# Optimization experiments

Hardware: AMD Instinct MI355X
Metric: run time of the kernel (lower is better)

The kernel has to match this reference:

```python
import jax, jax.numpy as jnp
import numpy as np


def _prelu(x, alpha):
    # PReLU with alpha shared over H,W (per-channel alpha, shape (C,))
    return jnp.where(x >= 0, x, alpha * x)


def _maxpool_2x2_s1_same(x):
    # TF MaxPooling2D(pool_size=2, strides=1, padding='same'): pad bottom/right
    return jax.lax.reduce_window(
        x, -jnp.inf, jax.lax.max,
        window_dimensions=(1, 2, 2, 1), window_strides=(1, 1, 1, 1),
        padding=[(0, 0), (0, 1), (0, 1), (0, 0)])


def _down_sample(x, W, b, alpha):
    # 1x1 Conv2D stride 2 'same' == subsample then channel matmul
    y = jnp.einsum('bhwc,cd->bhwd', x[:, ::2, ::2, :], W) + b
    y = _prelu(y, alpha)
    return _maxpool_2x2_s1_same(y)


def _up_sample(x, W, b, alpha):
    # 1x1 Conv2DTranspose stride 2 'same': even positions get conv output, rest only bias
    B, H, Wd, C = x.shape
    y = jnp.einsum('bhwc,cd->bhwd', x, W)
    z = jnp.zeros((B, 2 * H, 2 * Wd, C), dtype=x.dtype).at[:, ::2, ::2, :].set(y) + b
    z = _prelu(z, alpha)
    return _maxpool_2x2_s1_same(z)


def setup_inputs() -> dict:
    key = jax.random.key(0)
    ks = jax.random.split(key, 12)
    B, H, C = 8, 512, 3
    return {
        'input1': jax.random.normal(ks[0], (B, 2 * H, 2 * H, C), jnp.float32),
        'input2': jax.random.normal(ks[1], (B, H, H, C), jnp.float32),
        'input3': jax.random.normal(ks[2], (B, H // 2, H // 2, C), jnp.float32),
        'W_down': jax.random.normal(ks[3], (C, C), jnp.float32) * 0.5,
        'b_down': jax.random.normal(ks[4], (C,), jnp.float32) * 0.1,
        'alpha_down': jax.random.uniform(ks[5], (C,), jnp.float32) * 0.25,
        'W_up': jax.random.normal(ks[6], (C, C), jnp.float32) * 0.5,
        'b_up': jax.random.normal(ks[7], (C,), jnp.float32) * 0.1,
        'alpha_up': jax.random.uniform(ks[8], (C,), jnp.float32) * 0.25,
        'W_c': jax.random.normal(ks[9], (C, C), jnp.float32) * 0.5,
        'b_c': jax.random.normal(ks[10], (C,), jnp.float32) * 0.1,
        'alpha_g': jax.random.uniform(ks[11], (C,), jnp.float32) * 0.25,
        'scale': 2,
    }


def reference(input1, input2, input3, W_down, b_down, alpha_down,
              W_up, b_up, alpha_up, W_c, b_c, alpha_g, scale):
    assert scale == 2, 'only scale=2 path is well-defined in the source'
    i1 = _down_sample(input1, W_down, b_down, alpha_down)  # (B,H,W,C)
    i2 = input2
    i3 = _up_sample(input3, W_up, b_up, alpha_up)          # (B,H,W,C)

    s = i1 + i2 + i3
    g = jnp.mean(s, axis=(1, 2), keepdims=True)            # GlobalAvgPool, (B,1,1,C)

    conv1x1 = lambda t: jnp.einsum('bhwc,cd->bhwd', t, W_c) + b_c
    x = _prelu(conv1x1(g), alpha_g)
    # self.conv2d is the SAME layer applied three times -> c1 == c2 == c3,
    # hence y1 == y2 == y3; compute once (identical math).
    y = jax.nn.softmax(conv1x1(x), axis=-1)                # (B,1,1,C)
    return y * i1 + y * i2 + y * i3
```

## Files before the change

### kernel.cpp

```cpp
#include <hip/hip_runtime.h>

#define HW 512
#define D1_PITCH 197

__device__ __forceinline__ float prelu(float x, float a) { return x >= 0.f ? x : a * x; }

__global__ __launch_bounds__(256) void k1_compute_s(
    const float* __restrict__ in1, const float* __restrict__ in2, const float* __restrict__ in3,
    const float* __restrict__ Wd, const float* __restrict__ bd, const float* __restrict__ ad,
    const float* __restrict__ Wu, const float* __restrict__ bu, const float* __restrict__ au,
    float* __restrict__ s_out, float* __restrict__ partials)
{
    __shared__ float d1[17 * D1_PITCH];
    __shared__ float red[4][3];

    const int tid   = threadIdx.x;
    const int bx    = blockIdx.x;
    const int by    = blockIdx.y;
    const int batch = blockIdx.z;
    const int h0    = by * 16;
    const int w0b   = bx * 64;

    float wd[9], wu[9];
    #pragma unroll
    for (int k = 0; k < 9; k++) { wd[k] = Wd[k]; wu[k] = Wu[k]; }
    const float bd0 = bd[0], bd1 = bd[1], bd2 = bd[2];
    const float ad0 = ad[0], ad1 = ad[1], ad2 = ad[2];
    const float bu0 = bu[0], bu1 = bu[1], bu2 = bu[2];
    const float au0 = au[0], au1 = au[1], au2 = au[2];
    const float cu0 = prelu(bu0, au0), cu1 = prelu(bu1, au1), cu2 = prelu(bu2, au2);

    #pragma unroll
    for (int k = 0; k < 5; ++k) {
        const int e = k * 256 + tid;
        if (e < 17 * 65) {
            const int dr = e / 65, dc = e - dr * 65;
            const int gh = h0 + dr, gw = w0b + dc;
            float v0 = -INFINITY, v1 = -INFINITY, v2 = -INFINITY;
            if (gh < HW && gw < HW) {
                const float* p = in1 + ((size_t)((batch * 1024 + 2 * gh) * 1024 + 2 * gw)) * 3;
                const float x0 = p[0], x1 = p[1], x2 = p[2];
                v0 = prelu(x0 * wd[0] + x1 * wd[3] + x2 * wd[6] + bd0, ad0);
                v1 = prelu(x0 * wd[1] + x1 * wd[4] + x2 * wd[7] + bd1, ad1);
                v2 = prelu(x0 * wd[2] + x1 * wd[5] + x2 * wd[8] + bd2, ad2);
            }
            float* q = d1 + dr * D1_PITCH + dc * 3;
            q[0] = v0; q[1] = v1; q[2] = v2;
        }
    }
    __syncthreads();

    const int r  = tid >> 4;
    const int cg = tid & 15;
    const int h  = h0 + r;
    const int w0 = w0b + cg * 4;

    const float* in2p = in2 + ((size_t)((batch * HW + h) * HW + w0)) * 3;
    float i2v[12];
    #pragma unroll
    for (int k = 0; k < 3; ++k)
        *reinterpret_cast<float4*>(&i2v[4 * k]) = reinterpret_cast<const float4*>(in2p)[k];

    const int he = h + (h & 1);
    const bool heok = he < HW;
    const int w3 = w0 >> 1;
    float ud[3][3];
    #pragma unroll
    for (int k = 0; k < 3; ++k) {
        float u0 = cu0, u1 = cu1, u2 = cu2;
        if (heok && (w3 + k) < 256) {
            const float* p = in3 + ((size_t)((batch * 256 + (he >> 1)) * 256 + w3 + k)) * 3;
            const float x0 = p[0], x1 = p[1], x2 = p[2];
            u0 = fmaxf(u0, prelu(x0 * wu[0] + x1 * wu[3] + x2 * wu[6] + bu0, au0));
            u1 = fmaxf(u1, prelu(x0 * wu[1] + x1 * wu[4] + x2 * wu[7] + bu1, au1));
            u2 = fmaxf(u2, prelu(x0 * wu[2] + x1 * wu[5] + x2 * wu[8] + bu2, au2));
        }
        ud[k][0] = u0; ud[k][1] = u1; ud[k][2] = u2;
    }

    const int baseA = r * D1_PITCH + cg * 12;
    const int baseB = baseA + D1_PITCH;
    float pA0 = d1[baseA + 0], pA1 = d1[baseA + 1], pA2 = d1[baseA + 2];
    float pB0 = d1[baseB + 0], pB1 = d1[baseB + 1], pB2 = d1[baseB + 2];

    float s[4][3];
    float sum0 = 0.f, sum1 = 0.f, sum2 = 0.f;
    #pragma unroll
    for (int j = 0; j < 4; ++j) {
        const int o = 3 * (j + 1);
        const float cA0 = d1[baseA + o], cA1 = d1[baseA + o + 1], cA2 = d1[baseA + o + 2];
        const float cB0 = d1[baseB + o], cB1 = d1[baseB + o + 1], cB2 = d1[baseB + o + 2];
        const int uk = (j + 1) >> 1;
        const float s0 = fmaxf(fmaxf(pA0, cA0), fmaxf(pB0, cB0)) + i2v[3 * j + 0] + ud[uk][0];
        const float s1 = fmaxf(fmaxf(pA1, cA1), fmaxf(pB1, cB1)) + i2v[3 * j + 1] + ud[uk][1];
        const float s2 = fmaxf(fmaxf(pA2, cA2), fmaxf(pB2, cB2)) + i2v[3 * j + 2] + ud[uk][2];
        s[j][0] = s0; s[j][1] = s1; s[j][2] = s2;
        sum0 += s0; sum1 += s1; sum2 += s2;
        pA0 = cA0; pA1 = cA1; pA2 = cA2;
        pB0 = cB0; pB1 = cB1; pB2 = cB2;
    }

    float* outp = s_out + ((size_t)((batch * HW + h) * HW + w0)) * 3;
    #pragma unroll
    for (int k = 0; k < 3; ++k) {
        float4 v;
        v.x = s[(4 * k + 0) / 3][(4 * k + 0) % 3];
        v.y = s[(4 * k + 1) / 3][(4 * k + 1) % 3];
        v.z = s[(4 * k + 2) / 3][(4 * k + 2) % 3];
        v.w = s[(4 * k + 3) / 3][(4 * k + 3) % 3];
        reinterpret_cast<float4*>(outp)[k] = v;
    }

    #pragma unroll
    for (int off = 32; off > 0; off >>= 1) {
        sum0 += __shfl_down(sum0, off);
        sum1 += __shfl_down(sum1, off);
        sum2 += __shfl_down(sum2, off);
    }
    if ((tid & 63) == 0) { red[tid >> 6][0] = sum0; red[tid >> 6][1] = sum1; red[tid >> 6][2] = sum2; }
    __syncthreads();
    if (tid == 0) {
        const int pid = (batch * 32 + by) * 8 + bx;
        partials[pid * 3 + 0] = red[0][0] + red[1][0] + red[2][0] + red[3][0];
        partials[pid * 3 + 1] = red[0][1] + red[1][1] + red[2][1] + red[3][1];
        partials[pid * 3 + 2] = red[0][2] + red[1][2] + red[2][2] + red[3][2];
    }
}

__global__ __launch_bounds__(256) void k2_gate_scale(
    const float* __restrict__ partials,
    const float* __restrict__ Wc, const float* __restrict__ bc, const float* __restrict__ ag,
    float* __restrict__ out)
{
    __shared__ float ybuf[3];
    const int bid   = blockIdx.x;
    const int batch = bid >> 7;
    const int chunk = bid & 127;
    const int tid   = threadIdx.x;

    if (tid < 64) {
        const float* pw = partials + batch * 256 * 3;
        float g0 = 0.f, g1 = 0.f, g2 = 0.f;
        #pragma unroll
        for (int k = 0; k < 4; ++k) {
            const float* p = pw + (tid + 64 * k) * 3;
            g0 += p[0]; g1 += p[1]; g2 += p[2];
        }
        #pragma unroll
        for (int off = 32; off > 0; off >>= 1) {
            g0 += __shfl_down(g0, off);
            g1 += __shfl_down(g1, off);
            g2 += __shfl_down(g2, off);
        }
        if (tid == 0) {
            const float inv_n = 1.f / (float)(HW * HW);
            g0 *= inv_n; g1 *= inv_n; g2 *= inv_n;
            const float x0 = prelu(g0 * Wc[0] + g1 * Wc[3] + g2 * Wc[6] + bc[0], ag[0]);
            const float x1 = prelu(g0 * Wc[1] + g1 * Wc[4] + g2 * Wc[7] + bc[1], ag[1]);
            const float x2 = prelu(g0 * Wc[2] + g1 * Wc[5] + g2 * Wc[8] + bc[2], ag[2]);
            const float q0 = x0 * Wc[0] + x1 * Wc[3] + x2 * Wc[6] + bc[0];
            const float q1 = x0 * Wc[1] + x1 * Wc[4] + x2 * Wc[7] + bc[1];
            const float q2 = x0 * Wc[2] + x1 * Wc[5] + x2 * Wc[8] + bc[2];
            const float m  = fmaxf(q0, fmaxf(q1, q2));
            const float e0 = expf(q0 - m), e1 = expf(q1 - m), e2 = expf(q2 - m);
            const float inv = 1.f / (e0 + e1 + e2);
            ybuf[0] = e0 * inv; ybuf[1] = e1 * inv; ybuf[2] = e2 * inv;
        }
    }
    __syncthreads();
    const float ym[3] = { ybuf[0], ybuf[1], ybuf[2] };

    float* p = out + ((size_t)batch * 262144 + chunk * 2048 + tid * 8) * 3;
    #pragma unroll
    for (int k = 0; k < 6; ++k) {
        float4 v = reinterpret_cast<float4*>(p)[k];
        v.x *= ym[(4 * k + 0) % 3];
        v.y *= ym[(4 * k + 1) % 3];
        v.z *= ym[(4 * k + 2) % 3];
        v.w *= ym[(4 * k + 3) % 3];
        reinterpret_cast<float4*>(p)[k] = v;
    }
}

extern "C" void kernel_launch(void* const* d_in, const int* in_sizes, int n_in,
                              void* d_out, int out_size, void* d_ws, size_t ws_size,
                              hipStream_t stream)
{
    const float* in1 = (const float*)d_in[0];
    const float* in2 = (const float*)d_in[1];
    const float* in3 = (const float*)d_in[2];
    const float* Wd  = (const float*)d_in[3];
    const float* bd  = (const float*)d_in[4];
    const float* ad  = (const float*)d_in[5];
    const float* Wu  = (const float*)d_in[6];
    const float* bu  = (const float*)d_in[7];
    const float* au  = (const float*)d_in[8];
    const float* Wc  = (const float*)d_in[9];
    const float* bc  = (const float*)d_in[10];
    const float* ag  = (const float*)d_in[11];
    float* out = (float*)d_out;
    float* partials = (float*)d_ws;

    k1_compute_s<<<dim3(8, 32, 8), 256, 0, stream>>>(in1, in2, in3, Wd, bd, ad, Wu, bu, au, out, partials);
    k2_gate_scale<<<1024, 256, 0, stream>>>(partials, Wc, bc, ag, out);
}
```

Baseline: 42.67 us.

## Recompute intermediate sums in scale kernel instead of storing and reloading them

The first kernel now only produces per-block partial sums and no longer writes the full intermediate tensor. The second kernel recomputes the down/up-sample and sum on the same tiling, then multiplies by the softmax gate and writes the output once. This removes the write and reread of the intermediate, in exchange for reading the three inputs twice and doing the conv/pool arithmetic twice.

```diff
diff --git a/kernel.cpp b/kernel.cpp
--- a/kernel.cpp
+++ b/kernel.cpp
@@ -5,11 +5,12 @@
 
 __device__ __forceinline__ float prelu(float x, float a) { return x >= 0.f ? x : a * x; }
 
-__global__ __launch_bounds__(256) void k1_compute_s(
+
+__global__ __launch_bounds__(256) void k1_sums(
     const float* __restrict__ in1, const float* __restrict__ in2, const float* __restrict__ in3,
     const float* __restrict__ Wd, const float* __restrict__ bd, const float* __restrict__ ad,
     const float* __restrict__ Wu, const float* __restrict__ bu, const float* __restrict__ au,
-    float* __restrict__ s_out, float* __restrict__ partials)
+    float* __restrict__ partials)
 {
     __shared__ float d1[17 * D1_PITCH];
     __shared__ float red[4][3];
@@ -83,7 +84,6 @@
     float pA0 = d1[baseA + 0], pA1 = d1[baseA + 1], pA2 = d1[baseA + 2];
     float pB0 = d1[baseB + 0], pB1 = d1[baseB + 1], pB2 = d1[baseB + 2];
 
-    float s[4][3];
     float sum0 = 0.f, sum1 = 0.f, sum2 = 0.f;
     #pragma unroll
     for (int j = 0; j < 4; ++j) {
@@ -91,24 +91,11 @@
         const float cA0 = d1[baseA + o], cA1 = d1[baseA + o + 1], cA2 = d1[baseA + o + 2];
         const float cB0 = d1[baseB + o], cB1 = d1[baseB + o + 1], cB2 = d1[baseB + o + 2];
         const int uk = (j + 1) >> 1;
-        const float s0 = fmaxf(fmaxf(pA0, cA0), fmaxf(pB0, cB0)) + i2v[3 * j + 0] + ud[uk][0];
-        const float s1 = fmaxf(fmaxf(pA1, cA1), fmaxf(pB1, cB1)) + i2v[3 * j + 1] + ud[uk][1];
-        const float s2 = fmaxf(fmaxf(pA2, cA2), fmaxf(pB2, cB2)) + i2v[3 * j + 2] + ud[uk][2];
-        s[j][0] = s0; s[j][1] = s1; s[j][2] = s2;
-        sum0 += s0; sum1 += s1; sum2 += s2;
+        sum0 += fmaxf(fmaxf(pA0, cA0), fmaxf(pB0, cB0)) + i2v[3 * j + 0] + ud[uk][0];
+        sum1 += fmaxf(fmaxf(pA1, cA1), fmaxf(pB1, cB1)) + i2v[3 * j + 1] + ud[uk][1];
+        sum2 += fmaxf(fmaxf(pA2, cA2), fmaxf(pB2, cB2)) + i2v[3 * j + 2] + ud[uk][2];
         pA0 = cA0; pA1 = cA1; pA2 = cA2;
         pB0 = cB0; pB1 = cB1; pB2 = cB2;
-    }
-
-    float* outp = s_out + ((size_t)((batch * HW + h) * HW + w0)) * 3;
-    #pragma unroll
-    for (int k = 0; k < 3; ++k) {
-        float4 v;
-        v.x = s[(4 * k + 0) / 3][(4 * k + 0) % 3];
-        v.y = s[(4 * k + 1) / 3][(4 * k + 1) % 3];
-        v.z = s[(4 * k + 2) / 3][(4 * k + 2) % 3];
-        v.w = s[(4 * k + 3) / 3][(4 * k + 3) % 3];
-        reinterpret_cast<float4*>(outp)[k] = v;
     }
 
     #pragma unroll
@@ -127,16 +114,23 @@
     }
 }
 
-__global__ __launch_bounds__(256) void k2_gate_scale(
+__global__ __launch_bounds__(256) void k2_recompute_scale(
+    const float* __restrict__ in1, const float* __restrict__ in2, const float* __restrict__ in3,
+    const float* __restrict__ Wd, const float* __restrict__ bd, const float* __restrict__ ad,
+    const float* __restrict__ Wu, const float* __restrict__ bu, const float* __restrict__ au,
     const float* __restrict__ partials,
     const float* __restrict__ Wc, const float* __restrict__ bc, const float* __restrict__ ag,
     float* __restrict__ out)
 {
+    __shared__ float d1[17 * D1_PITCH];
     __shared__ float ybuf[3];
-    const int bid   = blockIdx.x;
-    const int batch = bid >> 7;
-    const int chunk = bid & 127;
+
     const int tid   = threadIdx.x;
+    const int bx    = blockIdx.x;
+    const int by    = blockIdx.y;
+    const int batch = blockIdx.z;
+    const int h0    = by * 16;
+    const int w0b   = bx * 64;
 
     if (tid < 64) {
         const float* pw = partials + batch * 256 * 3;
@@ -167,18 +161,93 @@
             ybuf[0] = e0 * inv; ybuf[1] = e1 * inv; ybuf[2] = e2 * inv;
         }
     }
+
+    float wd[9], wu[9];
+    #pragma unroll
+    for (int k = 0; k < 9; k++) { wd[k] = Wd[k]; wu[k] = Wu[k]; }
+    const float bd0 = bd[0], bd1 = bd[1], bd2 = bd[2];
+    const float ad0 = ad[0], ad1 = ad[1], ad2 = ad[2];
+    const float bu0 = bu[0], bu1 = bu[1], bu2 = bu[2];
+    const float au0 = au[0], au1 = au[1], au2 = au[2];
+    const float cu0 = prelu(bu0, au0), cu1 = prelu(bu1, au1), cu2 = prelu(bu2, au2);
+
+    #pragma unroll
+    for (int k = 0; k < 5; ++k) {
+        const int e = k * 256 + tid;
+        if (e < 17 * 65) {
+            const int dr = e / 65, dc = e - dr * 65;
+            const int gh = h0 + dr, gw = w0b + dc;
+            float v0 = -INFINITY, v1 = -INFINITY, v2 = -INFINITY;
+            if (gh < HW && gw < HW) {
+                const float* p = in1 + ((size_t)((batch * 1024 + 2 * gh) * 1024 + 2 * gw)) * 3;
+                const float x0 = p[0], x1 = p[1], x2 = p[2];
+                v0 = prelu(x0 * wd[0] + x1 * wd[3] + x2 * wd[6] + bd0, ad0);
+                v1 = prelu(x0 * wd[1] + x1 * wd[4] + x2 * wd[7] + bd1, ad1);
+                v2 = prelu(x0 * wd[2] + x1 * wd[5] + x2 * wd[8] + bd2, ad2);
+            }
+            float* q = d1 + dr * D1_PITCH + dc * 3;
+            q[0] = v0; q[1] = v1; q[2] = v2;
+        }
+    }
     __syncthreads();
+
+    const int r  = tid >> 4;
+    const int cg = tid & 15;
+    const int h  = h0 + r;
+    const int w0 = w0b + cg * 4;
+
+    const float* in2p = in2 + ((size_t)((batch * HW + h) * HW + w0)) * 3;
+    float i2v[12];
+    #pragma unroll
+    for (int k = 0; k < 3; ++k)
+        *reinterpret_cast<float4*>(&i2v[4 * k]) = reinterpret_cast<const float4*>(in2p)[k];
+
+    const int he = h + (h & 1);
+    const bool heok = he < HW;
+    const int w3 = w0 >> 1;
+    float ud[3][3];
+    #pragma unroll
+    for (int k = 0; k < 3; ++k) {
+        float u0 = cu0, u1 = cu1, u2 = cu2;
+        if (heok && (w3 + k) < 256) {
+            const float* p = in3 + ((size_t)((batch * 256 + (he >> 1)) * 256 + w3 + k)) * 3;
+            const float x0 = p[0], x1 = p[1], x2 = p[2];
+            u0 = fmaxf(u0, prelu(x0 * wu[0] + x1 * wu[3] + x2 * wu[6] + bu0, au0));
+            u1 = fmaxf(u1, prelu(x0 * wu[1] + x1 * wu[4] + x2 * wu[7] + bu1, au1));
+            u2 = fmaxf(u2, prelu(x0 * wu[2] + x1 * wu[5] + x2 * wu[8] + bu2, au2));
+        }
+        ud[k][0] = u0; ud[k][1] = u1; ud[k][2] = u2;
+    }
+
+    const int baseA = r * D1_PITCH + cg * 12;
+    const int baseB = baseA + D1_PITCH;
+    float pA0 = d1[baseA + 0], pA1 = d1[baseA + 1], pA2 = d1[baseA + 2];
+    float pB0 = d1[baseB + 0], pB1 = d1[baseB + 1], pB2 = d1[baseB + 2];
+
+    float s[4][3];
+    #pragma unroll
+    for (int j = 0; j < 4; ++j) {
+        const int o = 3 * (j + 1);
+        const float cA0 = d1[baseA + o], cA1 = d1[baseA + o + 1], cA2 = d1[baseA + o + 2];
+        const float cB0 = d1[baseB + o], cB1 = d1[baseB + o + 1], cB2 = d1[baseB + o + 2];
+        const int uk = (j + 1) >> 1;
+        s[j][0] = fmaxf(fmaxf(pA0, cA0), fmaxf(pB0, cB0)) + i2v[3 * j + 0] + ud[uk][0];
+        s[j][1] = fmaxf(fmaxf(pA1, cA1), fmaxf(pB1, cB1)) + i2v[3 * j + 1] + ud[uk][1];
+        s[j][2] = fmaxf(fmaxf(pA2, cA2), fmaxf(pB2, cB2)) + i2v[3 * j + 2] + ud[uk][2];
+        pA0 = cA0; pA1 = cA1; pA2 = cA2;
+        pB0 = cB0; pB1 = cB1; pB2 = cB2;
+    }
+
     const float ym[3] = { ybuf[0], ybuf[1], ybuf[2] };
-
-    float* p = out + ((size_t)batch * 262144 + chunk * 2048 + tid * 8) * 3;
-    #pragma unroll
-    for (int k = 0; k < 6; ++k) {
-        float4 v = reinterpret_cast<float4*>(p)[k];
-        v.x *= ym[(4 * k + 0) % 3];
-        v.y *= ym[(4 * k + 1) % 3];
-        v.z *= ym[(4 * k + 2) % 3];
-        v.w *= ym[(4 * k + 3) % 3];
-        reinterpret_cast<float4*>(p)[k] = v;
+    float* outp = out + ((size_t)((batch * HW + h) * HW + w0)) * 3;
+    #pragma unroll
+    for (int k = 0; k < 3; ++k) {
+        float4 v;
+        v.x = s[(4 * k + 0) / 3][(4 * k + 0) % 3] * ym[(4 * k + 0) % 3];
+        v.y = s[(4 * k + 1) / 3][(4 * k + 1) % 3] * ym[(4 * k + 1) % 3];
+        v.z = s[(4 * k + 2) / 3][(4 * k + 2) % 3] * ym[(4 * k + 2) % 3];
+        v.w = s[(4 * k + 3) / 3][(4 * k + 3) % 3] * ym[(4 * k + 3) % 3];
+        reinterpret_cast<float4*>(outp)[k] = v;
     }
 }
 
@@ -201,6 +270,7 @@
     float* out = (float*)d_out;
     float* partials = (float*)d_ws;
 
-    k1_compute_s<<<dim3(8, 32, 8), 256, 0, stream>>>(in1, in2, in3, Wd, bd, ad, Wu, bu, au, out, partials);
-    k2_gate_scale<<<1024, 256, 0, stream>>>(partials, Wc, bc, ag, out);
+    k1_sums<<<dim3(8, 32, 8), 256, 0, stream>>>(in1, in2, in3, Wd, bd, ad, Wu, bu, au, partials);
+    k2_recompute_scale<<<dim3(8, 32, 8), 256, 0, stream>>>(in1, in2, in3, Wd, bd, ad, Wu, bu, au,
+                                                           partials, Wc, bc, ag, out);
 }
```

Measured after the change: 42.95 us. No clear change (+0.6%).

## Recompute s in second pass instead of storing and rereading intermediate

Applied to the files above, without the earlier changes.

Replaces the store-s-then-rescale scheme with two passes of one templated kernel. Pass 0 computes only the per-block partial sums, and pass 1 recomputes s from the inputs and writes the gated output directly. This removes the intermediate write and the read-modify-write of the output, at the cost of reading in1/in2/in3 twice. It also switches in1 loads to vectorized float4 row loads with clamped indices instead of branches, and adds a launch-bounds occupancy hint.

```diff
diff --git a/kernel.cpp b/kernel.cpp
--- a/kernel.cpp
+++ b/kernel.cpp
@@ -1,18 +1,22 @@
 #include <hip/hip_runtime.h>
 
 #define HW 512
-#define D1_PITCH 197
+#define PITCH 200
 
 __device__ __forceinline__ float prelu(float x, float a) { return x >= 0.f ? x : a * x; }
 
-__global__ __launch_bounds__(256) void k1_compute_s(
+template<int MODE>
+__global__ __launch_bounds__(256, 4) void pass_kernel(
     const float* __restrict__ in1, const float* __restrict__ in2, const float* __restrict__ in3,
     const float* __restrict__ Wd, const float* __restrict__ bd, const float* __restrict__ ad,
     const float* __restrict__ Wu, const float* __restrict__ bu, const float* __restrict__ au,
-    float* __restrict__ s_out, float* __restrict__ partials)
+    float* __restrict__ partials,
+    const float* __restrict__ Wc, const float* __restrict__ bc, const float* __restrict__ ag,
+    float* __restrict__ out)
 {
-    __shared__ float d1[17 * D1_PITCH];
+    __shared__ float d1[17 * PITCH];
     __shared__ float red[4][3];
+    __shared__ float ybuf[3];
 
     const int tid   = threadIdx.x;
     const int bx    = blockIdx.x;
@@ -21,124 +25,7 @@
     const int h0    = by * 16;
     const int w0b   = bx * 64;
 
-    float wd[9], wu[9];
-    #pragma unroll
-    for (int k = 0; k < 9; k++) { wd[k] = Wd[k]; wu[k] = Wu[k]; }
-    const float bd0 = bd[0], bd1 = bd[1], bd2 = bd[2];
-    const float ad0 = ad[0], ad1 = ad[1], ad2 = ad[2];
-    const float bu0 = bu[0], bu1 = bu[1], bu2 = bu[2];
-    const float au0 = au[0], au1 = au[1], au2 = au[2];
-    const float cu0 = prelu(bu0, au0), cu1 = prelu(bu1, au1), cu2 = prelu(bu2, au2);
-
-    #pragma unroll
-    for (int k = 0; k < 5; ++k) {
-        const int e = k * 256 + tid;
-        if (e < 17 * 65) {
-            const int dr = e / 65, dc = e - dr * 65;
-            const int gh = h0 + dr, gw = w0b + dc;
-            float v0 = -INFINITY, v1 = -INFINITY, v2 = -INFINITY;
-            if (gh < HW && gw < HW) {
-                const float* p = in1 + ((size_t)((batch * 1024 + 2 * gh) * 1024 + 2 * gw)) * 3;
-                const float x0 = p[0], x1 = p[1], x2 = p[2];
-                v0 = prelu(x0 * wd[0] + x1 * wd[3] + x2 * wd[6] + bd0, ad0);
-                v1 = prelu(x0 * wd[1] + x1 * wd[4] + x2 * wd[7] + bd1, ad1);
-                v2 = prelu(x0 * wd[2] + x1 * wd[5] + x2 * wd[8] + bd2, ad2);
-            }
-            float* q = d1 + dr * D1_PITCH + dc * 3;
-            q[0] = v0; q[1] = v1; q[2] = v2;
-        }
-    }
-    __syncthreads();
-
-    const int r  = tid >> 4;
-    const int cg = tid & 15;
-    const int h  = h0 + r;
-    const int w0 = w0b + cg * 4;
-
-    const float* in2p = in2 + ((size_t)((batch * HW + h) * HW + w0)) * 3;
-    float i2v[12];
-    #pragma unroll
-    for (int k = 0; k < 3; ++k)
-        *reinterpret_cast<float4*>(&i2v[4 * k]) = reinterpret_cast<const float4*>(in2p)[k];
-
-    const int he = h + (h & 1);
-    const bool heok = he < HW;
-    const int w3 = w0 >> 1;
-    float ud[3][3];
-    #pragma unroll
-    for (int k = 0; k < 3; ++k) {
-        float u0 = cu0, u1 = cu1, u2 = cu2;
-        if (heok && (w3 + k) < 256) {
-            const float* p = in3 + ((size_t)((batch * 256 + (he >> 1)) * 256 + w3 + k)) * 3;
-            const float x0 = p[0], x1 = p[1], x2 = p[2];
-            u0 = fmaxf(u0, prelu(x0 * wu[0] + x1 * wu[3] + x2 * wu[6] + bu0, au0));
-            u1 = fmaxf(u1, prelu(x0 * wu[1] + x1 * wu[4] + x2 * wu[7] + bu1, au1));
-            u2 = fmaxf(u2, prelu(x0 * wu[2] + x1 * wu[5] + x2 * wu[8] + bu2, au2));
-        }
-        ud[k][0] = u0; ud[k][1] = u1; ud[k][2] = u2;
-    }
-
-    const int baseA = r * D1_PITCH + cg * 12;
-    const int baseB = baseA + D1_PITCH;
-    float pA0 = d1[baseA + 0], pA1 = d1[baseA + 1], pA2 = d1[baseA + 2];
-    float pB0 = d1[baseB + 0], pB1 = d1[baseB + 1], pB2 = d1[baseB + 2];
-
-    float s[4][3];
-    float sum0 = 0.f, sum1 = 0.f, sum2 = 0.f;
-    #pragma unroll
-    for (int j = 0; j < 4; ++j) {
-        const int o = 3 * (j + 1);
-        const float cA0 = d1[baseA + o], cA1 = d1[baseA + o + 1], cA2 = d1[baseA + o + 2];
-        const float cB0 = d1[baseB + o], cB1 = d1[baseB + o + 1], cB2 = d1[baseB + o + 2];
-        const int uk = (j + 1) >> 1;
-        const float s0 = fmaxf(fmaxf(pA0, cA0), fmaxf(pB0, cB0)) + i2v[3 * j + 0] + ud[uk][0];
-        const float s1 = fmaxf(fmaxf(pA1, cA1), fmaxf(pB1, cB1)) + i2v[3 * j + 1] + ud[uk][1];
-        const float s2 = fmaxf(fmaxf(pA2, cA2), fmaxf(pB2, cB2)) + i2v[3 * j + 2] + ud[uk][2];
-        s[j][0] = s0; s[j][1] = s1; s[j][2] = s2;
-        sum0 += s0; sum1 += s1; sum2 += s2;
-        pA0 = cA0; pA1 = cA1; pA2 = cA2;
-        pB0 = cB0; pB1 = cB1; pB2 = cB2;
-    }
-
-    float* outp = s_out + ((size_t)((batch * HW + h) * HW + w0)) * 3;
-    #pragma unroll
-    for (int k = 0; k < 3; ++k) {
-        float4 v;
-        v.x = s[(4 * k + 0) / 3][(4 * k + 0) % 3];
-        v.y = s[(4 * k + 1) / 3][(4 * k + 1) % 3];
-        v.z = s[(4 * k + 2) / 3][(4 * k + 2) % 3];
-        v.w = s[(4 * k + 3) / 3][(4 * k + 3) % 3];
-        reinterpret_cast<float4*>(outp)[k] = v;
-    }
-
-    #pragma unroll
-    for (int off = 32; off > 0; off >>= 1) {
-        sum0 += __shfl_down(sum0, off);
-        sum1 += __shfl_down(sum1, off);
-        sum2 += __shfl_down(sum2, off);
-    }
-    if ((tid & 63) == 0) { red[tid >> 6][0] = sum0; red[tid >> 6][1] = sum1; red[tid >> 6][2] = sum2; }
-    __syncthreads();
-    if (tid == 0) {
-        const int pid = (batch * 32 + by) * 8 + bx;
-        partials[pid * 3 + 0] = red[0][0] + red[1][0] + red[2][0] + red[3][0];
-        partials[pid * 3 + 1] = red[0][1] + red[1][1] + red[2][1] + red[3][1];
-        partials[pid * 3 + 2] = red[0][2] + red[1][2] + red[2][2] + red[3][2];
-    }
-}
-
-__global__ __launch_bounds__(256) void k2_gate_scale(
-    const float* __restrict__ partials,
-    const float* __restrict__ Wc, const float* __restrict__ bc, const float* __restrict__ ag,
-    float* __restrict__ out)
-{
-    __shared__ float ybuf[3];
-    const int bid   = blockIdx.x;
-    const int batch = bid >> 7;
-    const int chunk = bid & 127;
-    const int tid   = threadIdx.x;
-
-    if (tid < 64) {
+    if (MODE == 1 && tid < 64) {
         const float* pw = partials + batch * 256 * 3;
         float g0 = 0.f, g1 = 0.f, g2 = 0.f;
         #pragma unroll
@@ -167,18 +54,141 @@
             ybuf[0] = e0 * inv; ybuf[1] = e1 * inv; ybuf[2] = e2 * inv;
         }
     }
+
+    float wd[9], wu[9];
+    #pragma unroll
+    for (int k = 0; k < 9; k++) { wd[k] = Wd[k]; wu[k] = Wu[k]; }
+    const float bd0 = bd[0], bd1 = bd[1], bd2 = bd[2];
+    const float ad0 = ad[0], ad1 = ad[1], ad2 = ad[2];
+    const float bu0 = bu[0], bu1 = bu[1], bu2 = bu[2];
+    const float au0 = au[0], au1 = au[1], au2 = au[2];
+    const float cu0 = prelu(bu0, au0), cu1 = prelu(bu1, au1), cu2 = prelu(bu2, au2);
+
+    #pragma unroll
+    for (int step = 0; step < 2; ++step) {
+        const int r = step ? 16 : (tid >> 4);
+        const int g = step ? tid : (tid & 15);
+        if (step == 0 || tid < 16) {
+            const int gh  = h0 + r;
+            const int ghc = gh < HW ? gh : (HW - 1);
+            const float* rb = in1 + ((size_t)(batch * 1024 + 2 * ghc)) * 3072;
+            const int px0 = 2 * w0b + 8 * g;
+            const float4* lp = reinterpret_cast<const float4*>(rb + (size_t)px0 * 3);
+            float arr[28];
+            #pragma unroll
+            for (int k = 0; k < 7; ++k)
+                *reinterpret_cast<float4*>(&arr[4 * k]) = lp[k];
+
+            const bool rowOOR = (gh >= HW);
+            float* q = d1 + r * PITCH + 12 * g;
+            #pragma unroll
+            for (int j = 0; j < 4; ++j) {
+                const float x0 = arr[6 * j], x1 = arr[6 * j + 1], x2 = arr[6 * j + 2];
+                float v0 = prelu(x0 * wd[0] + x1 * wd[3] + x2 * wd[6] + bd0, ad0);
+                float v1 = prelu(x0 * wd[1] + x1 * wd[4] + x2 * wd[7] + bd1, ad1);
+                float v2 = prelu(x0 * wd[2] + x1 * wd[5] + x2 * wd[8] + bd2, ad2);
+                q[3 * j + 0] = rowOOR ? -INFINITY : v0;
+                q[3 * j + 1] = rowOOR ? -INFINITY : v1;
+                q[3 * j + 2] = rowOOR ? -INFINITY : v2;
+            }
+            if (g == 15) {
+                const float x0 = arr[24], x1 = arr[25], x2 = arr[26];
+                float v0 = prelu(x0 * wd[0] + x1 * wd[3] + x2 * wd[6] + bd0, ad0);
+                float v1 = prelu(x0 * wd[1] + x1 * wd[4] + x2 * wd[7] + bd1, ad1);
+                float v2 = prelu(x0 * wd[2] + x1 * wd[5] + x2 * wd[8] + bd2, ad2);
+                const bool oor = rowOOR || (w0b + 64 >= HW);
+                q[12] = oor ? -INFINITY : v0;
+                q[13] = oor ? -INFINITY : v1;
+                q[14] = oor ? -INFINITY : v2;
+            }
+        }
+    }
     __syncthreads();
-    const float ym[3] = { ybuf[0], ybuf[1], ybuf[2] };
-
-    float* p = out + ((size_t)batch * 262144 + chunk * 2048 + tid * 8) * 3;
-    #pragma unroll
-    for (int k = 0; k < 6; ++k) {
-        float4 v = reinterpret_cast<float4*>(p)[k];
-        v.x *= ym[(4 * k + 0) % 3];
-        v.y *= ym[(4 * k + 1) % 3];
-        v.z *= ym[(4 * k + 2) % 3];
-        v.w *= ym[(4 * k + 3) % 3];
-        reinterpret_cast<float4*>(p)[k] = v;
+
+    const int r  = tid >> 4;
+    const int cg = tid & 15;
+    const int h  = h0 + r;
+    const int w0 = w0b + cg * 4;
+
+    const float* in2p = in2 + ((size_t)((batch * HW + h) * HW + w0)) * 3;
+    float i2v[12];
+    #pragma unroll
+    for (int k = 0; k < 3; ++k)
+        *reinterpret_cast<float4*>(&i2v[4 * k]) = reinterpret_cast<const float4*>(in2p)[k];
+
+    const int he  = h + (h & 1);
+    const bool rOK = he < HW;
+    const int hr3 = rOK ? (he >> 1) : 255;
+    const int w3  = w0 >> 1;
+    float ur[9];
+    #pragma unroll
+    for (int k = 0; k < 3; ++k) {
+        const int wc = (w3 + k < 256) ? (w3 + k) : 255;
+        const float* p = in3 + ((size_t)(batch * 256 + hr3) * 256 + wc) * 3;
+        ur[3 * k + 0] = p[0]; ur[3 * k + 1] = p[1]; ur[3 * k + 2] = p[2];
+    }
+    float ud[3][3];
+    #pragma unroll
+    for (int k = 0; k < 3; ++k) {
+        const bool ok = rOK && (w3 + k < 256);
+        const float x0 = ur[3 * k], x1 = ur[3 * k + 1], x2 = ur[3 * k + 2];
+        const float u0 = prelu(x0 * wu[0] + x1 * wu[3] + x2 * wu[6] + bu0, au0);
+        const float u1 = prelu(x0 * wu[1] + x1 * wu[4] + x2 * wu[7] + bu1, au1);
+        const float u2 = prelu(x0 * wu[2] + x1 * wu[5] + x2 * wu[8] + bu2, au2);
+        ud[k][0] = ok ? fmaxf(cu0, u0) : cu0;
+        ud[k][1] = ok ? fmaxf(cu1, u1) : cu1;
+        ud[k][2] = ok ? fmaxf(cu2, u2) : cu2;
+    }
+
+    const int baseA = r * PITCH + cg * 12;
+    const int baseB = baseA + PITCH;
+    float pA0 = d1[baseA + 0], pA1 = d1[baseA + 1], pA2 = d1[baseA + 2];
+    float pB0 = d1[baseB + 0], pB1 = d1[baseB + 1], pB2 = d1[baseB + 2];
+
+    float s[4][3];
+    #pragma unroll
+    for (int j = 0; j < 4; ++j) {
+        const int o = 3 * (j + 1);
+        const float cA0 = d1[baseA + o], cA1 = d1[baseA + o + 1], cA2 = d1[baseA + o + 2];
+        const float cB0 = d1[baseB + o], cB1 = d1[baseB + o + 1], cB2 = d1[baseB + o + 2];
+        const int uk = (j + 1) >> 1;
+        s[j][0] = fmaxf(fmaxf(pA0, cA0), fmaxf(pB0, cB0)) + i2v[3 * j + 0] + ud[uk][0];
+        s[j][1] = fmaxf(fmaxf(pA1, cA1), fmaxf(pB1, cB1)) + i2v[3 * j + 1] + ud[uk][1];
+        s[j][2] = fmaxf(fmaxf(pA2, cA2), fmaxf(pB2, cB2)) + i2v[3 * j + 2] + ud[uk][2];
+        pA0 = cA0; pA1 = cA1; pA2 = cA2;
+        pB0 = cB0; pB1 = cB1; pB2 = cB2;
+    }
+
+    if (MODE == 0) {
+        float sum0 = s[0][0] + s[1][0] + s[2][0] + s[3][0];
+        float sum1 = s[0][1] + s[1][1] + s[2][1] + s[3][1];
+        float sum2 = s[0][2] + s[1][2] + s[2][2] + s[3][2];
+        #pragma unroll
+        for (int off = 32; off > 0; off >>= 1) {
+            sum0 += __shfl_down(sum0, off);
+            sum1 += __shfl_down(sum1, off);
+            sum2 += __shfl_down(sum2, off);
+        }
+        if ((tid & 63) == 0) { red[tid >> 6][0] = sum0; red[tid >> 6][1] = sum1; red[tid >> 6][2] = sum2; }
+        __syncthreads();
+        if (tid == 0) {
+            const int pid = (batch * 32 + by) * 8 + bx;
+            partials[pid * 3 + 0] = red[0][0] + red[1][0] + red[2][0] + red[3][0];
+            partials[pid * 3 + 1] = red[0][1] + red[1][1] + red[2][1] + red[3][1];
+            partials[pid * 3 + 2] = red[0][2] + red[1][2] + red[2][2] + red[3][2];
+        }
+    } else {
+        const float ym[3] = { ybuf[0], ybuf[1], ybuf[2] };
+        float* outp = out + ((size_t)((batch * HW + h) * HW + w0)) * 3;
+        #pragma unroll
+        for (int k = 0; k < 3; ++k) {
+            float4 v;
+            v.x = s[(4 * k + 0) / 3][(4 * k + 0) % 3] * ym[(4 * k + 0) % 3];
+            v.y = s[(4 * k + 1) / 3][(4 * k + 1) % 3] * ym[(4 * k + 1) % 3];
+            v.z = s[(4 * k + 2) / 3][(4 * k + 2) % 3] * ym[(4 * k + 2) % 3];
+            v.w = s[(4 * k + 3) / 3][(4 * k + 3) % 3] * ym[(4 * k + 3) % 3];
+            reinterpret_cast<float4*>(outp)[k] = v;
+        }
     }
 }
 
@@ -201,6 +211,8 @@
     float* out = (float*)d_out;
     float* partials = (float*)d_ws;
 
-    k1_compute_s<<<dim3(8, 32, 8), 256, 0, stream>>>(in1, in2, in3, Wd, bd, ad, Wu, bu, au, out, partials);
-    k2_gate_scale<<<1024, 256, 0, stream>>>(partials, Wc, bc, ag, out);
+    pass_kernel<0><<<dim3(8, 32, 8), 256, 0, stream>>>(in1, in2, in3, Wd, bd, ad, Wu, bu, au,
+                                                       partials, Wc, bc, ag, out);
+    pass_kernel<1><<<dim3(8, 32, 8), 256, 0, stream>>>(in1, in2, in3, Wd, bd, ad, Wu, bu, au,
+                                                       partials, Wc, bc, ag, out);
 }
```

Result: faster. 38.96 us (-8.7%).
